# Kernel optimization log

Measured on AMD Instinct MI355X. Metric: run time of the kernel, lower is better.

The kernel has to match this reference:

```python
import jax, jax.numpy as jnp
import numpy as np

NUM_HEADS = 12
MAX_DIST = 127  # table side = 2*MAX_DIST+1 = 255


def _relative_position_index(H, W):
    # Static (numpy) computation of the Swin-style relative position index.
    coords = np.stack(np.meshgrid(np.arange(H), np.arange(W), indexing='ij'))  # (2,H,W)
    coords = coords.reshape(2, -1)                      # (2, N)
    rel = coords[:, :, None] - coords[:, None, :]       # (2, N, N)
    rel = rel.transpose(1, 2, 0).astype(np.int64)       # (N, N, 2)
    rel[..., 0] += H - 1
    rel[..., 1] += W - 1
    rel[..., 0] *= 2 * W - 1
    return rel.sum(-1)                                  # (N, N)


def setup_inputs() -> dict:
    key = jax.random.key(0)
    k1, k2, k3, k4 = jax.random.split(key, 4)
    B, N, C = 8, 1024, 768
    table_size = (2 * MAX_DIST + 1) ** 2  # 65025
    return {
        'x': jax.random.normal(k1, (B, N, C), dtype=jnp.float32),
        'qkv_w': jax.random.normal(k2, (C, 3 * C), dtype=jnp.float32) * 0.02,
        'proj_w': jax.random.normal(k3, (C, C), dtype=jnp.float32) * 0.02,
        'proj_b': jnp.zeros((C,), dtype=jnp.float32),
        'bias_table': jax.random.normal(k4, (table_size, NUM_HEADS), dtype=jnp.float32) * 0.02,
    }


def reference(x, qkv_w, proj_w, proj_b, bias_table):
    B, N, C = x.shape
    H = W = int(N ** 0.5)
    nh = NUM_HEADS
    hd = C // nh
    scale = hd ** -0.5

    qkv = (x @ qkv_w).reshape(B, N, 3, nh, hd)
    qkv = jnp.transpose(qkv, (2, 0, 3, 1, 4))  # (3, B, nh, N, hd)
    q, k, v = qkv[0], qkv[1], qkv[2]

    attn = jnp.einsum('bhnd,bhmd->bhnm', q, k) * scale  # (B, nh, N, N)

    idx = jnp.asarray(_relative_position_index(H, W))   # (N, N) static
    bias = bias_table[idx.reshape(-1)].reshape(N, N, nh)
    bias = jnp.transpose(bias, (2, 0, 1))                # (nh, N, N)
    attn = attn + bias[None]

    attn = jax.nn.softmax(attn, axis=-1)
    out = jnp.einsum('bhnm,bhmd->bhnd', attn, v)         # (B, nh, N, hd)
    out = jnp.transpose(out, (0, 2, 1, 3)).reshape(B, N, C)
    return out @ proj_w + proj_b
```

## Files before the change

### kernel.cpp

```cpp
#include <hip/hip_runtime.h>

typedef unsigned short u16;
typedef __attribute__((ext_vector_type(8))) short bf16x8;
typedef __attribute__((ext_vector_type(4))) short s16x4;
typedef __attribute__((ext_vector_type(4))) float f32x4;
typedef __attribute__((ext_vector_type(16))) float f32x16;

#define MFMA(a, b, c) __builtin_amdgcn_mfma_f32_16x16x32_bf16(a, b, c, 0, 0, 0)
#define MFMA32(a, b, c) __builtin_amdgcn_mfma_f32_32x32x16_bf16(a, b, c, 0, 0, 0)

#define GLDS16(gp, lp)                                                        \
  __builtin_amdgcn_global_load_lds(                                          \
      (__attribute__((address_space(1))) void*)(void*)(gp),                  \
      (__attribute__((address_space(3))) void*)(lp), 16, 0, 0)

__device__ __forceinline__ u16 f2b(float f) {
  union { float f; unsigned u; } x; x.f = f;
  unsigned r = x.u + 0x7fffu + ((x.u >> 16) & 1u);
  return (u16)(r >> 16);
}
__device__ __forceinline__ float b2f(u16 v) {
  union { unsigned u; float f; } x; x.u = ((unsigned)v) << 16;
  return x.f;
}
__device__ __forceinline__ unsigned cvtpk(float a, float b) {
  unsigned r;
  asm("v_cvt_pk_bf16_f32 %0, %1, %2" : "=v"(r) : "v"(a), "v"(b));
  return r;
}
__device__ __forceinline__ void pl32swap(unsigned& a, unsigned& b) {
  asm volatile("v_permlane32_swap_b32 %0, %1" : "+v"(a), "+v"(b));
}

template <int NPASS>
__device__ __forceinline__ void stage64(const u16* __restrict__ src, int ld,
                                        u16* lds, int t) {
  int wave = t >> 6;
#pragma unroll
  for (int p = 0; p < NPASS; ++p) {
    int row = p * 32 + (t >> 3);
    int ss = (t & 7) ^ (row & 7);
    const u16* g = src + row * ld + ss * 8;
    GLDS16(g, lds + (p * 2048 + wave * 512));
  }
}

__device__ __forceinline__ bf16x8 ldsfrag(const u16* base, int row, int slot) {
  int byte = row * 128 + (((slot) ^ (row & 7)) << 4);
  return *(const bf16x8*)((const char*)base + byte);
}

__global__ void cast_x_kernel(const float* __restrict__ in, u16* __restrict__ out,
                              int n4) {
  int i = blockIdx.x * blockDim.x + threadIdx.x;
  if (i < n4) {
    float4 v = ((const float4*)in)[i];
    ushort4 o;
    o.x = f2b(v.x); o.y = f2b(v.y); o.z = f2b(v.z); o.w = f2b(v.w);
    ((ushort4*)out)[i] = o;
  }
}

__global__ void transpose_cast(const float* __restrict__ in, u16* __restrict__ out,
                               int R, int Ccols) {
  __shared__ u16 tile[32][33];
  int c0 = blockIdx.x * 32, r0 = blockIdx.y * 32;
  int tx = threadIdx.x & 31, ty = threadIdx.x >> 5;
#pragma unroll
  for (int rr = ty; rr < 32; rr += 8)
    tile[rr][tx] = f2b(in[(size_t)(r0 + rr) * Ccols + c0 + tx]);
  __syncthreads();
#pragma unroll
  for (int rr = ty; rr < 32; rr += 8)
    out[(size_t)(c0 + rr) * R + r0 + tx] = tile[tx][rr];
}

__global__ void gather_bias(const float* __restrict__ btab, u16* __restrict__ out) {
  int i = blockIdx.x * 256 + threadIdx.x;
  int p = i & 31, q = (i >> 5) & 31, dy = (i >> 10) % 63, h = i / (63 * 1024);
  int hi = p >> 4, e = p & 15;
  int j31 = (e & 3) + 8 * (e >> 2) + 4 * hi;
  int dx = q + 31 - j31;
  out[i] = f2b(btab[(dy * 63 + dx) * 12 + h] * 1.44269504f);
}

template <int EPI>
__global__ __launch_bounds__(256, 3) void gemm128(
    const u16* __restrict__ A, const u16* __restrict__ BT, int K, int NT,
    u16* __restrict__ qo, u16* __restrict__ ko, u16* __restrict__ vo,
    const float* __restrict__ pb, float* __restrict__ out, int Nld) {
  __shared__ __align__(16) u16 As[128 * 64];
  __shared__ __align__(16) u16 Bs[128 * 64];
  const int t = threadIdx.x;
  const int wave = t >> 6, lane = t & 63;
  const int wr = wave >> 1, wc = wave & 1;
  const int cpx = gridDim.x >> 3;
  const int id = blockIdx.x;
  const int sw = (id & 7) * cpx + (id >> 3);
  const int trow = sw / NT;
  const int tileRow = trow * 128, tileCol = (sw - trow * NT) * 128;
  const u16* Ab = A + (size_t)tileRow * K;
  const u16* Bb = BT + (size_t)tileCol * K;

  f32x4 acc[4][4] = {};
  for (int k0 = 0; k0 < K; k0 += 64) {
    __syncthreads();
    stage64<4>(Ab + k0, K, As, t);
    stage64<4>(Bb + k0, K, Bs, t);
    __syncthreads();
#pragma unroll
    for (int kk = 0; kk < 2; ++kk) {
      bf16x8 af[4], bfr[4];
#pragma unroll
      for (int m = 0; m < 4; ++m)
        af[m] = ldsfrag(As, wr * 64 + m * 16 + (lane & 15), kk * 4 + (lane >> 4));
#pragma unroll
      for (int n = 0; n < 4; ++n)
        bfr[n] = ldsfrag(Bs, wc * 64 + n * 16 + (lane & 15), kk * 4 + (lane >> 4));
#pragma unroll
      for (int m = 0; m < 4; ++m)
#pragma unroll
        for (int n = 0; n < 4; ++n)
          acc[m][n] = MFMA(af[m], bfr[n], acc[m][n]);
    }
  }

  if (EPI == 0) {
    const int which = tileCol / 768;
    const int cb = tileCol - which * 768;
    if (which == 0) {
#pragma unroll
      for (int m = 0; m < 4; ++m)
#pragma unroll
        for (int n = 0; n < 4; ++n) {
          int c = cb + wc * 64 + n * 16 + (lane & 15);
          int hh = c >> 6, d = c & 63;
#pragma unroll
          for (int r = 0; r < 4; ++r) {
            int row = tileRow + wr * 64 + m * 16 + (lane >> 4) * 4 + r;
            int bb = row >> 10, nn = row & 1023;
            qo[((size_t)(bb * 12 + hh) * 1024 + nn) * 64 + d] =
                f2b(acc[m][n][r] * 0.18033688f);
          }
        }
    } else if (which == 1) {
#pragma unroll
      for (int m = 0; m < 4; ++m)
#pragma unroll
        for (int n = 0; n < 4; ++n) {
          int c = cb + wc * 64 + n * 16 + (lane & 15);
          int hh = c >> 6, d = c & 63;
#pragma unroll
          for (int r = 0; r < 4; ++r) {
            int row = tileRow + wr * 64 + m * 16 + (lane >> 4) * 4 + r;
            int bb = row >> 10, nn = row & 1023;
            ko[((size_t)(bb * 12 + hh) * 1024 + nn) * 64 + d] =
                f2b(acc[m][n][r]);
          }
        }
    } else {
#pragma unroll
      for (int m = 0; m < 4; ++m)
#pragma unroll
        for (int n = 0; n < 4; ++n) {
          int c = cb + wc * 64 + n * 16 + (lane & 15);
          int hh = c >> 6, d = c & 63;
          int rowb = tileRow + wr * 64 + m * 16 + (lane >> 4) * 4;
          int bb = rowb >> 10, nn = rowb & 1023;
          union { unsigned u[2]; s16x4 v; } w;
          w.u[0] = cvtpk(acc[m][n][0], acc[m][n][1]);
          w.u[1] = cvtpk(acc[m][n][2], acc[m][n][3]);
          *(s16x4*)(vo + (((size_t)(bb * 12 + hh) * 64 + d) * 1024 + nn)) = w.v;
        }
    }
  } else {
#pragma unroll
    for (int m = 0; m < 4; ++m)
#pragma unroll
      for (int n = 0; n < 4; ++n) {
        int col = tileCol + wc * 64 + n * 16 + (lane & 15);
#pragma unroll
        for (int r = 0; r < 4; ++r) {
          int row = tileRow + wr * 64 + m * 16 + (lane >> 4) * 4 + r;
          out[(size_t)row * Nld + col] = acc[m][n][r] + pb[col];
        }
      }
  }
}

__global__ __launch_bounds__(256, 3) void attn_kernel(
    const u16* __restrict__ qm, const u16* __restrict__ kmat,
    const u16* __restrict__ vT, const u16* __restrict__ biasx,
    u16* __restrict__ ao) {
  __shared__ __align__(16) u16 Ks[2][64 * 64];
  __shared__ __align__(16) u16 Vs[2][64 * 64];

  const int t = threadIdx.x;
  const int wv = t >> 6, lane = t & 63;
  const int hi = lane >> 5, q = lane & 31;
  const int id = blockIdx.x;
  const int sw = (id & 7) * 96 + (id >> 3);
  const int qt = sw & 7, h = (sw >> 3) % 12, b = sw / 96;
  const int bh = b * 12 + h;

  const u16* kb0 = kmat + (size_t)bh * 1024 * 64;
  const u16* vb0 = vT + (size_t)bh * 64 * 1024;
  const u16* bx0 = biasx + (((size_t)h * 63) * 32 + q) * 32 + hi * 16;

  const u16* qb = qm + ((size_t)bh * 1024 + qt * 128 + wv * 32) * 64;
  bf16x8 qf[4];
#pragma unroll
  for (int dblk = 0; dblk < 4; ++dblk)
    qf[dblk] = *(const bf16x8*)(qb + q * 64 + dblk * 16 + hi * 8);

  f32x16 o32[2] = {};
  float mrun = -1e30f, lrun = 0.f;

  const int ldy0 = wv + qt * 4 + 31;

  for (int kt8 = 0; kt8 < 8; ++kt8) {
    __syncthreads();
    stage64<2>(kb0 + kt8 * 8192, 64, Ks[0], t);
    stage64<2>(kb0 + kt8 * 8192 + 4096, 64, Ks[1], t);
    stage64<2>(vb0 + kt8 * 128, 1024, Vs[0], t);
    stage64<2>(vb0 + kt8 * 128 + 64, 1024, Vs[1], t);

    bf16x8 bb[4][2];
#pragma unroll
    for (int kb = 0; kb < 4; ++kb) {
      const u16* bp = bx0 + (size_t)(ldy0 - kt8 * 4 - kb) * 1024;
      bb[kb][0] = *(const bf16x8*)(bp);
      bb[kb][1] = *(const bf16x8*)(bp + 8);
    }
    __syncthreads();

    f32x16 s4[4] = {};
#pragma unroll
    for (int kb = 0; kb < 4; ++kb) {
      const u16* Kc = Ks[kb >> 1];
      int krow = (kb & 1) * 32 + q;
#pragma unroll
      for (int dblk = 0; dblk < 4; ++dblk) {
        bf16x8 kf = ldsfrag(Kc, krow, dblk * 2 + hi);
        s4[kb] = MFMA32(kf, qf[dblk], s4[kb]);
      }
    }

#pragma unroll
    for (int kb = 0; kb < 4; ++kb)
#pragma unroll
      for (int e = 0; e < 16; ++e)
        s4[kb][e] += b2f((u16)(e < 8 ? bb[kb][0][e] : bb[kb][1][e - 8]));

    float mx = -1e30f;
#pragma unroll
    for (int kb = 0; kb < 4; ++kb)
#pragma unroll
      for (int e = 0; e < 16; ++e) mx = fmaxf(mx, s4[kb][e]);

    if (__any(mx > mrun + 11.5f)) {
      float mf = fmaxf(mx, __shfl_xor(mx, 32));
      float mn = fmaxf(mrun, mf);
      float al = __builtin_amdgcn_exp2f(mrun - mn);
      mrun = mn;
      lrun *= al;
#pragma unroll
      for (int e = 0; e < 16; ++e) {
        int qr = (e & 3) + 8 * (e >> 2) + 4 * hi;
        float ar = __shfl(al, qr);
        o32[0][e] *= ar;
        o32[1][e] *= ar;
      }
    }

#pragma unroll
    for (int kb = 0; kb < 4; ++kb)
#pragma unroll
      for (int e = 0; e < 16; ++e) {
        float p = __builtin_amdgcn_exp2f(s4[kb][e] - mrun);
        s4[kb][e] = p;
        lrun += p;
      }

#pragma unroll
    for (int kb = 0; kb < 4; ++kb) {
      const f32x16& sv = s4[kb];
      unsigned w[8];
#pragma unroll
      for (int m = 0; m < 8; ++m) w[m] = cvtpk(sv[2 * m], sv[2 * m + 1]);
      pl32swap(w[0], w[2]);
      pl32swap(w[1], w[3]);
      pl32swap(w[4], w[6]);
      pl32swap(w[5], w[7]);
      const u16* Vc = Vs[kb >> 1];
#pragma unroll
      for (int kk16 = 0; kk16 < 2; ++kk16) {
        union { unsigned u[4]; bf16x8 v; } pa;
        pa.u[0] = w[kk16 * 4 + 0];
        pa.u[1] = w[kk16 * 4 + 1];
        pa.u[2] = w[kk16 * 4 + 2];
        pa.u[3] = w[kk16 * 4 + 3];
        int slot16 = (kb & 1) * 2 + kk16;
#pragma unroll
        for (int dblk = 0; dblk < 2; ++dblk) {
          bf16x8 vf = ldsfrag(Vc, dblk * 32 + q, slot16 * 2 + hi);
          o32[dblk] = MFMA32(pa.v, vf, o32[dblk]);
        }
      }
    }
  }

  lrun += __shfl_xor(lrun, 32);
#pragma unroll
  for (int e = 0; e < 16; ++e) {
    int qr = (e & 3) + 8 * (e >> 2) + 4 * hi;
    float lv = __builtin_amdgcn_rcpf(__shfl(lrun, qr));
    int i = qt * 128 + wv * 32 + qr;
#pragma unroll
    for (int dblk = 0; dblk < 2; ++dblk) {
      int d = dblk * 32 + q;
      float val = o32[dblk][e] * lv;
      ao[((size_t)b * 1024 + i) * 768 + h * 64 + d] = f2b(val);
    }
  }
}

extern "C" void kernel_launch(void* const* d_in, const int* in_sizes, int n_in,
                              void* d_out, int out_size, void* d_ws, size_t ws_size,
                              hipStream_t stream) {
  const float* x = (const float*)d_in[0];
  const float* qkvw = (const float*)d_in[1];
  const float* projw = (const float*)d_in[2];
  const float* projb = (const float*)d_in[3];
  const float* btab = (const float*)d_in[4];
  float* out = (float*)d_out;
  char* ws = (char*)d_ws;

  u16* xb = (u16*)(ws);
  u16* wqkvT = (u16*)(ws + 12582912);
  u16* wprojT = (u16*)(ws + 16121856);
  u16* qbuf = (u16*)(ws + 17301504);
  u16* kbuf = (u16*)(ws + 29884416);
  u16* vTbuf = (u16*)(ws + 42467328);
  u16* biasx = (u16*)(ws + 55050240);
  u16* ao = xb;

  cast_x_kernel<<<6144, 256, 0, stream>>>(x, xb, 8192 * 768 / 4);
  transpose_cast<<<dim3(72, 24), 256, 0, stream>>>(qkvw, wqkvT, 768, 2304);
  transpose_cast<<<dim3(24, 24), 256, 0, stream>>>(projw, wprojT, 768, 768);
  gather_bias<<<3024, 256, 0, stream>>>(btab, biasx);

  gemm128<0><<<1152, 256, 0, stream>>>(xb, wqkvT, 768, 18, qbuf, kbuf,
                                       vTbuf, nullptr, nullptr, 0);

  attn_kernel<<<768, 256, 0, stream>>>(qbuf, kbuf, vTbuf, biasx, ao);

  gemm128<1><<<384, 256, 0, stream>>>(ao, wprojT, 768, 6, nullptr, nullptr,
                                      nullptr, projb, out, 768);
}
```

Measured before the change: 125.9 us.

## Store bias as fp32 and preload it into MFMA accumulators

The precomputed relative-position bias is now kept in fp32 instead of bf16 and loaded straight into the score accumulators before the QK^T MFMAs. This removes the separate bf16-to-fp32 unpack and add pass over the 64 scores. The max reduction is rewritten as a tree and the exp-sum uses four partial accumulators to shorten dependency chains. In exchange, the bias load per tile doubles in bytes and the bias buffer doubles in size.

```diff
diff --git a/kernel.cpp b/kernel.cpp
--- a/kernel.cpp
+++ b/kernel.cpp
@@ -18,10 +18,6 @@
   union { float f; unsigned u; } x; x.f = f;
   unsigned r = x.u + 0x7fffu + ((x.u >> 16) & 1u);
   return (u16)(r >> 16);
-}
-__device__ __forceinline__ float b2f(u16 v) {
-  union { unsigned u; float f; } x; x.u = ((unsigned)v) << 16;
-  return x.f;
 }
 __device__ __forceinline__ unsigned cvtpk(float a, float b) {
   unsigned r;
@@ -75,13 +71,13 @@
     out[(size_t)(c0 + rr) * R + r0 + tx] = tile[tx][rr];
 }
 
-__global__ void gather_bias(const float* __restrict__ btab, u16* __restrict__ out) {
+__global__ void gather_bias(const float* __restrict__ btab, float* __restrict__ out) {
   int i = blockIdx.x * 256 + threadIdx.x;
   int p = i & 31, q = (i >> 5) & 31, dy = (i >> 10) % 63, h = i / (63 * 1024);
   int hi = p >> 4, e = p & 15;
   int j31 = (e & 3) + 8 * (e >> 2) + 4 * hi;
   int dx = q + 31 - j31;
-  out[i] = f2b(btab[(dy * 63 + dx) * 12 + h] * 1.44269504f);
+  out[i] = btab[(dy * 63 + dx) * 12 + h] * 1.44269504f;
 }
 
 template <int EPI>
@@ -190,7 +186,7 @@
 
 __global__ __launch_bounds__(256, 3) void attn_kernel(
     const u16* __restrict__ qm, const u16* __restrict__ kmat,
-    const u16* __restrict__ vT, const u16* __restrict__ biasx,
+    const u16* __restrict__ vT, const float* __restrict__ biasx,
     u16* __restrict__ ao) {
   __shared__ __align__(16) u16 Ks[2][64 * 64];
   __shared__ __align__(16) u16 Vs[2][64 * 64];
@@ -205,7 +201,7 @@
 
   const u16* kb0 = kmat + (size_t)bh * 1024 * 64;
   const u16* vb0 = vT + (size_t)bh * 64 * 1024;
-  const u16* bx0 = biasx + (((size_t)h * 63) * 32 + q) * 32 + hi * 16;
+  const float* bx0 = biasx + (((size_t)h * 63) * 32 + q) * 32 + hi * 16;
 
   const u16* qb = qm + ((size_t)bh * 1024 + qt * 128 + wv * 32) * 64;
   bf16x8 qf[4];
@@ -225,16 +221,21 @@
     stage64<2>(vb0 + kt8 * 128, 1024, Vs[0], t);
     stage64<2>(vb0 + kt8 * 128 + 64, 1024, Vs[1], t);
 
-    bf16x8 bb[4][2];
-#pragma unroll
-    for (int kb = 0; kb < 4; ++kb) {
-      const u16* bp = bx0 + (size_t)(ldy0 - kt8 * 4 - kb) * 1024;
-      bb[kb][0] = *(const bf16x8*)(bp);
-      bb[kb][1] = *(const bf16x8*)(bp + 8);
+    f32x16 s4[4];
+#pragma unroll
+    for (int kb = 0; kb < 4; ++kb) {
+      const float* bp = bx0 + (size_t)(ldy0 - kt8 * 4 - kb) * 1024;
+#pragma unroll
+      for (int e4 = 0; e4 < 4; ++e4) {
+        f32x4 bv = *(const f32x4*)(bp + e4 * 4);
+        s4[kb][e4 * 4 + 0] = bv[0];
+        s4[kb][e4 * 4 + 1] = bv[1];
+        s4[kb][e4 * 4 + 2] = bv[2];
+        s4[kb][e4 * 4 + 3] = bv[3];
+      }
     }
     __syncthreads();
 
-    f32x16 s4[4] = {};
 #pragma unroll
     for (int kb = 0; kb < 4; ++kb) {
       const u16* Kc = Ks[kb >> 1];
@@ -246,17 +247,16 @@
       }
     }
 
-#pragma unroll
-    for (int kb = 0; kb < 4; ++kb)
-#pragma unroll
-      for (int e = 0; e < 16; ++e)
-        s4[kb][e] += b2f((u16)(e < 8 ? bb[kb][0][e] : bb[kb][1][e - 8]));
-
     float mx = -1e30f;
 #pragma unroll
-    for (int kb = 0; kb < 4; ++kb)
-#pragma unroll
-      for (int e = 0; e < 16; ++e) mx = fmaxf(mx, s4[kb][e]);
+    for (int kb = 0; kb < 4; ++kb) {
+      const f32x16& sv = s4[kb];
+      float a0 = fmaxf(fmaxf(sv[0], sv[1]), fmaxf(sv[2], sv[3]));
+      float a1 = fmaxf(fmaxf(sv[4], sv[5]), fmaxf(sv[6], sv[7]));
+      float a2 = fmaxf(fmaxf(sv[8], sv[9]), fmaxf(sv[10], sv[11]));
+      float a3 = fmaxf(fmaxf(sv[12], sv[13]), fmaxf(sv[14], sv[15]));
+      mx = fmaxf(mx, fmaxf(fmaxf(a0, a1), fmaxf(a2, a3)));
+    }
 
     if (__any(mx > mrun + 11.5f)) {
       float mf = fmaxf(mx, __shfl_xor(mx, 32));
@@ -273,14 +273,21 @@
       }
     }
 
-#pragma unroll
-    for (int kb = 0; kb < 4; ++kb)
-#pragma unroll
-      for (int e = 0; e < 16; ++e) {
-        float p = __builtin_amdgcn_exp2f(s4[kb][e] - mrun);
-        s4[kb][e] = p;
-        lrun += p;
-      }
+    float ps0 = 0.f, ps1 = 0.f, ps2 = 0.f, ps3 = 0.f;
+#pragma unroll
+    for (int kb = 0; kb < 4; ++kb) {
+#pragma unroll
+      for (int e = 0; e < 16; e += 4) {
+        float p0 = __builtin_amdgcn_exp2f(s4[kb][e + 0] - mrun);
+        float p1 = __builtin_amdgcn_exp2f(s4[kb][e + 1] - mrun);
+        float p2 = __builtin_amdgcn_exp2f(s4[kb][e + 2] - mrun);
+        float p3 = __builtin_amdgcn_exp2f(s4[kb][e + 3] - mrun);
+        s4[kb][e + 0] = p0; s4[kb][e + 1] = p1;
+        s4[kb][e + 2] = p2; s4[kb][e + 3] = p3;
+        ps0 += p0; ps1 += p1; ps2 += p2; ps3 += p3;
+      }
+    }
+    lrun += (ps0 + ps1) + (ps2 + ps3);
 
 #pragma unroll
     for (int kb = 0; kb < 4; ++kb) {
@@ -342,7 +349,7 @@
   u16* qbuf = (u16*)(ws + 17301504);
   u16* kbuf = (u16*)(ws + 29884416);
   u16* vTbuf = (u16*)(ws + 42467328);
-  u16* biasx = (u16*)(ws + 55050240);
+  float* biasx = (float*)(ws + 55050240);
   u16* ao = xb;
 
   cast_x_kernel<<<6144, 256, 0, stream>>>(x, xb, 8192 * 768 / 4);
```

After: 140.6 us. 11.6% more time.
